# Kernel tuning notes

Measured on AMD Instinct MI355X. Metric: run time of the kernel, lower is better.

## Reference

```python
import jax, jax.numpy as jnp
import numpy as np

B, Te, Td, D_ENC, D_DEC, ATT = 8, 512, 128, 512, 512, 256


def setup_inputs() -> dict:
    key = jax.random.key(0)
    k0, k1, k2, k3, k4 = jax.random.split(key, 5)
    return {
        "values": jax.random.normal(k0, (B, Te, D_ENC), dtype=jnp.float32),
        "query": jax.random.normal(k1, (B, Td, D_DEC), dtype=jnp.float32),
        "W_h": jax.random.uniform(k2, (D_ENC, ATT), jnp.float32, -0.05, 0.05),
        "U_a": jax.random.uniform(k3, (D_DEC, ATT), jnp.float32, -0.05, 0.05),
        "V_a": jax.random.uniform(k4, (1, ATT), jnp.float32, -0.05, 0.05),
    }


def reference(values, query, W_h, U_a, V_a):
    # values: [B, Te, D_ENC] encoder output sequence (single entry in 'values' list)
    # query:  [B, Td, D_DEC] decoder output sequence
    # With a single encoder sequence, broadcast_sum/broadcast_concat reduces are identities.
    W_hi = jnp.einsum('bse,ea->bsa', values, W_h)        # [B, Te, ATT]
    U_a_dot_s = jnp.einsum('btd,da->bta', query, U_a)    # [B, Td, ATT]
    # tanh(h.Wa + s.Ua): vectorized over all decoder timesteps (K.rnn scan unrolled)
    act = jnp.tanh(W_hi[:, None, :, :] + U_a_dot_s[:, :, None, :])  # [B, Td, Te, ATT]
    scores = jnp.einsum('btsa,a->bts', act, V_a[0])      # [B, Td, Te]
    e_outputs = jax.nn.softmax(scores, axis=-1)          # softmax over encoder positions
    # context: weighted sum of encoder hidden states
    c_outputs = jnp.einsum('bts,bse->bte', e_outputs, values)  # [B, Td, D_ENC]
    return (c_outputs, e_outputs)
```

## Files before the change

### kernel.cpp

```cpp
#include <hip/hip_runtime.h>
#include <hip/hip_bf16.h>


typedef __attribute__((ext_vector_type(8))) short bf16x8;
typedef __attribute__((ext_vector_type(4))) float f32x4;

__device__ inline void f32_to_bf16_pair(float x, short& h, short& l) {
    unsigned u = __builtin_bit_cast(unsigned, x);
    unsigned r = u + 0x7FFFu + ((u >> 16) & 1u);
    h = (short)(r >> 16);
    float xh = __builtin_bit_cast(float, r & 0xFFFF0000u);
    float xl = x - xh;
    unsigned u2 = __builtin_bit_cast(unsigned, xl);
    unsigned r2 = u2 + 0x7FFFu + ((u2 >> 16) & 1u);
    l = (short)(r2 >> 16);
}

__global__ __launch_bounds__(256) void prep(
    const float* __restrict__ W_h, const float* __restrict__ U_a,
    const float* __restrict__ values, const float* __restrict__ query,
    short* __restrict__ BHi, short* __restrict__ BLo,
    short* __restrict__ AHi, short* __restrict__ ALo)
{
    __shared__ float TW[64][65];
    __shared__ float TA[16][516];
    const int bid = blockIdx.x;
    const int tid = threadIdx.x;

    if (bid < 64) {
        const int mat = bid >> 5, nb = (bid >> 3) & 3, kb = bid & 7;
        const float* W = mat ? U_a : W_h;
        {
            const int krow = tid >> 2, cq = (tid & 3) * 16;
            const float* src = W + (size_t)(kb * 64 + krow) * 256 + nb * 64 + cq;
            #pragma unroll
            for (int q = 0; q < 4; ++q)
                *(float4*)&TW[krow][cq + q * 4] = *(const float4*)&src[q * 4];
        }
        __syncthreads();
        {
            const int f = tid >> 5;
            const int ngl = f >> 1, ksl = f & 1;
            const int l0 = (tid & 31) * 2;
            const int ngrp = nb * 4 + ngl;
            const int ksg = kb * 2 + ksl;
            const size_t base = (size_t)mat * 131072 + ((size_t)(ngrp * 16 + ksg)) * 512;
            #pragma unroll
            for (int li = 0; li < 2; ++li) {
                const int lane = l0 + li;
                const int lr = lane & 15, lg = lane >> 4;
                bf16x8 hv, lv;
                #pragma unroll
                for (int j = 0; j < 8; ++j) {
                    short h, l;
                    f32_to_bf16_pair(TW[ksl * 32 + lg * 8 + j][ngl * 16 + lr], h, l);
                    hv[j] = h; lv[j] = l;
                }
                *(bf16x8*)(BHi + base + lane * 8) = hv;
                *(bf16x8*)(BLo + base + lane * 8) = lv;
            }
        }
    } else {
        const int mg = bid - 64;
        const float* src = (mg < 256) ? values + (size_t)mg * 16 * 512
                                      : query + (size_t)(mg - 256) * 16 * 512;
        {
            const int row = tid >> 4, c0 = (tid & 15) * 4;
            #pragma unroll
            for (int i = 0; i < 8; ++i)
                *(float4*)&TA[row][c0 + i * 64] =
                    *(const float4*)&src[(size_t)row * 512 + c0 + i * 64];
        }
        __syncthreads();
        {
            const int ks = tid >> 4;
            const int l4 = (tid & 15) * 4;
            const size_t base = ((size_t)(mg * 16 + ks)) * 512;
            #pragma unroll
            for (int li = 0; li < 4; ++li) {
                const int lane = l4 + li;
                const int lr = lane & 15, lg = lane >> 4;
                bf16x8 hv, lv;
                #pragma unroll
                for (int j = 0; j < 8; ++j) {
                    short h, l;
                    f32_to_bf16_pair(TA[lr][ks * 32 + lg * 8 + j], h, l);
                    hv[j] = h; lv[j] = l;
                }
                *(bf16x8*)(AHi + base + lane * 8) = hv;
                *(bf16x8*)(ALo + base + lane * 8) = lv;
            }
        }
    }
}

__global__ __launch_bounds__(128) void gemm_mfma(
    const short* __restrict__ AHi, const short* __restrict__ ALo,
    const short* __restrict__ BHi, const short* __restrict__ BLo,
    float* __restrict__ WhO, float* __restrict__ UO)
{
    const int bid = blockIdx.x;
    const int mt = bid >> 2, nt = bid & 3;
    const int tid = threadIdx.x;
    const int w = tid >> 6, l = tid & 63;
    const int lr = l & 15, lg = l >> 4;

    float* C; int m0, mg, matoff;
    if (mt < 128) { C = WhO; m0 = mt * 32; mg = mt * 2 + w; matoff = 0; }
    else { C = UO; m0 = (mt - 128) * 32; mg = 256 + (mt - 128) * 2 + w; matoff = 131072; }

    const short* ah_p = AHi + ((size_t)mg * 16) * 512 + l * 8;
    const short* al_p = ALo + ((size_t)mg * 16) * 512 + l * 8;
    const short* bh_p = BHi + matoff + ((size_t)(nt * 4) * 16) * 512 + l * 8;
    const short* bl_p = BLo + matoff + ((size_t)(nt * 4) * 16) * 512 + l * 8;

    f32x4 acc[4];
    #pragma unroll
    for (int nc = 0; nc < 4; ++nc) acc[nc] = (f32x4){0.f, 0.f, 0.f, 0.f};

    #pragma unroll 2
    for (int ks = 0; ks < 16; ++ks) {
        bf16x8 ah = *(const bf16x8*)(ah_p + (size_t)ks * 512);
        bf16x8 al = *(const bf16x8*)(al_p + (size_t)ks * 512);
        #pragma unroll
        for (int nc = 0; nc < 4; ++nc) {
            bf16x8 bh = *(const bf16x8*)(bh_p + ((size_t)(nc * 16 + ks)) * 512);
            bf16x8 bl = *(const bf16x8*)(bl_p + ((size_t)(nc * 16 + ks)) * 512);
            acc[nc] = __builtin_amdgcn_mfma_f32_16x16x32_bf16(ah, bh, acc[nc], 0, 0, 0);
            acc[nc] = __builtin_amdgcn_mfma_f32_16x16x32_bf16(al, bh, acc[nc], 0, 0, 0);
            acc[nc] = __builtin_amdgcn_mfma_f32_16x16x32_bf16(ah, bl, acc[nc], 0, 0, 0);
        }
    }

    const float SCL = 2.8853900817779268f;
    float* cp = C + (size_t)(m0 + w * 16 + lg * 4) * 256 + nt * 64 + lr;
    #pragma unroll
    for (int nc = 0; nc < 4; ++nc)
        #pragma unroll
        for (int r = 0; r < 4; ++r)
            cp[(size_t)r * 256 + nc * 16] = acc[nc][r] * SCL;
}

__global__ __launch_bounds__(256) void scores_k(
    const float* __restrict__ Whl, const float* __restrict__ Ul,
    const float* __restrict__ Va, float* __restrict__ scoresP)
{
    __shared__ float Ws[64][68];
    __shared__ float Us[16][68];

    const int bid = blockIdx.x;
    const int b = bid & 7;
    const int rest = bid >> 3;
    const int ah = rest & 3;
    const int tt = (rest >> 2) & 7;
    const int st = rest >> 5;
    const int t0 = tt * 16, s0 = st * 64, a0 = ah * 64;
    const int tid = threadIdx.x;

    {
        const int r = tid >> 2, c16 = (tid & 3) * 16;
        const float* wsrc = Whl + (size_t)(b * 512 + s0 + r) * 256 + a0 + c16;
        #pragma unroll
        for (int q = 0; q < 4; ++q)
            *(float4*)&Ws[r][c16 + q * 4] = *(const float4*)&wsrc[q * 4];
        const int r8 = tid >> 4, c8 = (tid & 15) * 4;
        const float* usrc = Ul + (size_t)(b * 128 + t0 + r8) * 256 + a0 + c8;
        *(float4*)&Us[r8][c8] = *(const float4*)&usrc[0];
    }
    __syncthreads();

    const int t = tid >> 4;
    const int ss = tid & 15;
    const float* Vp = Va + a0;

    float acc[4] = {};
    #pragma unroll 4
    for (int a = 0; a < 64; a += 4) {
        float4 u  = *(const float4*)&Us[t][a];
        float4 w0 = *(const float4*)&Ws[ss][a];
        float4 w1 = *(const float4*)&Ws[ss + 16][a];
        float4 w2 = *(const float4*)&Ws[ss + 32][a];
        float4 w3 = *(const float4*)&Ws[ss + 48][a];
        const float uv[4] = {u.x, u.y, u.z, u.w};
        const float wv[4][4] = {{w0.x, w0.y, w0.z, w0.w}, {w1.x, w1.y, w1.z, w1.w},
                                {w2.x, w2.y, w2.z, w2.w}, {w3.x, w3.y, w3.z, w3.w}};
        #pragma unroll
        for (int q = 0; q < 4; ++q) {
            const float vq = Vp[a + q];
            #pragma unroll
            for (int k = 0; k < 4; ++k) {
                float e = __builtin_amdgcn_exp2f(wv[k][q] + uv[q]);
                float r = __builtin_amdgcn_rcpf(1.f + e);
                acc[k] = fmaf(vq, r, acc[k]);
            }
        }
    }

    float* sp = scoresP + (size_t)ah * 524288
              + (size_t)(b * 128 + t0 + t) * 512 + s0 + ss;
    #pragma unroll
    for (int k = 0; k < 4; ++k) sp[k * 16] = acc[k];
}

__global__ __launch_bounds__(512) void softmax_ctx(
    const float* __restrict__ scoresP, const float* __restrict__ values,
    float* __restrict__ out_c, float* __restrict__ out_e)
{
    __shared__ float Ps[4][512];
    __shared__ float Part[7][4][256];

    const int bid = blockIdx.x;
    const int b = bid & 7;
    const int rest = bid >> 3;
    const int tg = rest & 31;
    const int eh = rest >> 5;
    const int t0 = tg * 4;
    const int tid = threadIdx.x;

    if (tid < 256) {
        const int row = tid >> 6, lane = tid & 63;
        const float* sp = scoresP + (size_t)(b * 128 + t0 + row) * 512;
        float e[8]; float ssum = 0.f;
        #pragma unroll
        for (int k = 0; k < 8; ++k) {
            const int idx = k * 64 + lane;
            float s = sp[idx] + sp[524288 + idx] + sp[1048576 + idx] + sp[1572864 + idx];
            e[k] = __builtin_amdgcn_exp2f(s * -2.8853900817779268f);
            ssum += e[k];
        }
        #pragma unroll
        for (int off = 32; off > 0; off >>= 1)
            ssum += __shfl_xor(ssum, off);
        const float inv = 1.0f / ssum;
        float* erow = out_e + (size_t)(b * 128 + t0 + row) * 512;
        #pragma unroll
        for (int k = 0; k < 8; ++k) {
            float p = e[k] * inv;
            Ps[row][k * 64 + lane] = p;
            if (eh == 0) erow[k * 64 + lane] = p;
        }
    }
    __syncthreads();

    const int el = (tid & 63) * 4;
    const int e4 = eh * 256 + el;
    const int sh = tid >> 6;
    const int sb = sh * 64;
    const float* vb = values + (size_t)b * 262144;

    float4 a0 = {0,0,0,0}, a1 = {0,0,0,0}, a2 = {0,0,0,0}, a3 = {0,0,0,0};
    #pragma unroll 2
    for (int s2 = 0; s2 < 64; s2 += 4) {
        float4 q0 = *(const float4*)&Ps[0][sb + s2];
        float4 q1 = *(const float4*)&Ps[1][sb + s2];
        float4 q2 = *(const float4*)&Ps[2][sb + s2];
        float4 q3 = *(const float4*)&Ps[3][sb + s2];
        const float q0v[4] = {q0.x, q0.y, q0.z, q0.w};
        const float q1v[4] = {q1.x, q1.y, q1.z, q1.w};
        const float q2v[4] = {q2.x, q2.y, q2.z, q2.w};
        const float q3v[4] = {q3.x, q3.y, q3.z, q3.w};
        #pragma unroll
        for (int j = 0; j < 4; ++j) {
            float4 v4 = *(const float4*)&vb[(size_t)(sb + s2 + j) * 512 + e4];
            a0.x = fmaf(q0v[j], v4.x, a0.x); a0.y = fmaf(q0v[j], v4.y, a0.y);
            a0.z = fmaf(q0v[j], v4.z, a0.z); a0.w = fmaf(q0v[j], v4.w, a0.w);
            a1.x = fmaf(q1v[j], v4.x, a1.x); a1.y = fmaf(q1v[j], v4.y, a1.y);
            a1.z = fmaf(q1v[j], v4.z, a1.z); a1.w = fmaf(q1v[j], v4.w, a1.w);
            a2.x = fmaf(q2v[j], v4.x, a2.x); a2.y = fmaf(q2v[j], v4.y, a2.y);
            a2.z = fmaf(q2v[j], v4.z, a2.z); a2.w = fmaf(q2v[j], v4.w, a2.w);
            a3.x = fmaf(q3v[j], v4.x, a3.x); a3.y = fmaf(q3v[j], v4.y, a3.y);
            a3.z = fmaf(q3v[j], v4.z, a3.z); a3.w = fmaf(q3v[j], v4.w, a3.w);
        }
    }

    if (sh) {
        *(float4*)&Part[sh - 1][0][el] = a0;
        *(float4*)&Part[sh - 1][1][el] = a1;
        *(float4*)&Part[sh - 1][2][el] = a2;
        *(float4*)&Part[sh - 1][3][el] = a3;
    }
    __syncthreads();
    if (!sh) {
        #pragma unroll
        for (int rrow = 0; rrow < 4; ++rrow) {
            float4 acc = (rrow == 0) ? a0 : (rrow == 1) ? a1 : (rrow == 2) ? a2 : a3;
            #pragma unroll
            for (int g = 0; g < 7; ++g) {
                float4 p4 = *(const float4*)&Part[g][rrow][el];
                acc.x += p4.x; acc.y += p4.y; acc.z += p4.z; acc.w += p4.w;
            }
            *(float4*)&out_c[(size_t)(b * 128 + t0 + rrow) * 512 + e4] = acc;
        }
    }
}

extern "C" void kernel_launch(void* const* d_in, const int* in_sizes, int n_in,
                              void* d_out, int out_size, void* d_ws, size_t ws_size,
                              hipStream_t stream) {
    const float* values = (const float*)d_in[0];
    const float* query  = (const float*)d_in[1];
    const float* W_h    = (const float*)d_in[2];
    const float* U_a    = (const float*)d_in[3];
    const float* V_a    = (const float*)d_in[4];

    float* ws      = (float*)d_ws;
    float* Whl     = ws;
    float* Ul      = ws + 1048576;
    float* scoresP = ws + 1310720;
    short* S       = (short*)(ws + 3407872);
    short* AHi     = S;
    short* ALo     = S + 2621440;
    short* BHi     = S + 5242880;
    short* BLo     = S + 5505024;

    float* out_c = (float*)d_out;
    float* out_e = out_c + 8 * 128 * 512;

    hipLaunchKernelGGL(prep, dim3(384), dim3(256), 0, stream,
                       W_h, U_a, values, query, BHi, BLo, AHi, ALo);
    hipLaunchKernelGGL(gemm_mfma, dim3(640), dim3(128), 0, stream,
                       AHi, ALo, BHi, BLo, Whl, Ul);
    hipLaunchKernelGGL(scores_k, dim3(2048), dim3(256), 0, stream,
                       Whl, Ul, V_a, scoresP);
    hipLaunchKernelGGL(softmax_ctx, dim3(512), dim3(512), 0, stream,
                       scoresP, values, out_c, out_e);
}
```

Measured before the change: 64.76 us.

## Fuse pipeline into cooperative persistent kernel and split A operand inside GEMM

Merges the four kernels into one cooperative persistent kernel with grid-wide syncs between phases, and falls back to separate launches if the cooperative launch fails. The GEMM no longer reads a prepacked bf16 hi/lo copy of values and query. It double-buffers the fp32 A tile through shared memory and splits it into bf16 hi/lo in registers with truncation, which removes the prep pass and its workspace traffic. The softmax-context phase now runs with 256 threads over half-width column slices across 1024 items. The change risks grid.sync overhead, lower occupancy from the union shared-memory footprint, and slightly different rounding from the truncating split.

Result: slower. 241.6 us (+273.1%).

```diff
diff --git a/kernel.cpp b/kernel.cpp
--- a/kernel.cpp
+++ b/kernel.cpp
@@ -1,5 +1,8 @@
 #include <hip/hip_runtime.h>
 #include <hip/hip_bf16.h>
+#include <hip/hip_cooperative_groups.h>
+
+namespace cg = cooperative_groups;
 
 
 typedef __attribute__((ext_vector_type(8))) short bf16x8;
@@ -16,120 +19,123 @@
     l = (short)(r2 >> 16);
 }
 
-__global__ __launch_bounds__(256) void prep(
+__device__ inline void split_trunc(float x, short& h, short& l) {
+    unsigned u = __builtin_bit_cast(unsigned, x);
+    h = (short)(u >> 16);
+    float xh = __builtin_bit_cast(float, u & 0xFFFF0000u);
+    unsigned u2 = __builtin_bit_cast(unsigned, x - xh);
+    l = (short)(u2 >> 16);
+}
+
+struct PwS { float TW[64][65]; };
+struct GmS { float As[2][64][68]; };
+struct ScS { float Ws[64][68]; float Us[16][68]; };
+struct SxS { float Ps[4][512]; float Part[7][4][128]; };
+union Smem { PwS pw; GmS gm; ScS sc; SxS sx; };
+
+__device__ void phase_prepB(int item, int tid, PwS& sm,
     const float* __restrict__ W_h, const float* __restrict__ U_a,
+    short* __restrict__ BHi, short* __restrict__ BLo)
+{
+    const int mat = item >> 5, nb = (item >> 3) & 3, kb = item & 7;
+    const float* W = mat ? U_a : W_h;
+    const int krow = tid >> 2, cq = (tid & 3) * 16;
+    const float* src = W + (size_t)(kb * 64 + krow) * 256 + nb * 64 + cq;
+    #pragma unroll
+    for (int q = 0; q < 4; ++q)
+        *(float4*)&sm.TW[krow][cq + q * 4] = *(const float4*)&src[q * 4];
+    __syncthreads();
+    const int f = tid >> 5;
+    const int ngl = f >> 1, ksl = f & 1;
+    const int l0 = (tid & 31) * 2;
+    const int ngrp = nb * 4 + ngl;
+    const int ksg = kb * 2 + ksl;
+    const size_t base = (size_t)mat * 131072 + (size_t)(ngrp * 16 + ksg) * 512;
+    #pragma unroll
+    for (int li = 0; li < 2; ++li) {
+        const int lane = l0 + li;
+        const int lr = lane & 15, lg = lane >> 4;
+        bf16x8 hv, lv;
+        #pragma unroll
+        for (int j = 0; j < 8; ++j) {
+            short h, l;
+            f32_to_bf16_pair(sm.TW[ksl * 32 + lg * 8 + j][ngl * 16 + lr], h, l);
+            hv[j] = h; lv[j] = l;
+        }
+        *(bf16x8*)(BHi + base + lane * 8) = hv;
+        *(bf16x8*)(BLo + base + lane * 8) = lv;
+    }
+    __syncthreads();
+}
+
+__device__ void phase_gemm(int item, int tid, GmS& sm,
     const float* __restrict__ values, const float* __restrict__ query,
-    short* __restrict__ BHi, short* __restrict__ BLo,
-    short* __restrict__ AHi, short* __restrict__ ALo)
-{
-    __shared__ float TW[64][65];
-    __shared__ float TA[16][516];
-    const int bid = blockIdx.x;
-    const int tid = threadIdx.x;
-
-    if (bid < 64) {
-        const int mat = bid >> 5, nb = (bid >> 3) & 3, kb = bid & 7;
-        const float* W = mat ? U_a : W_h;
-        {
-            const int krow = tid >> 2, cq = (tid & 3) * 16;
-            const float* src = W + (size_t)(kb * 64 + krow) * 256 + nb * 64 + cq;
-            #pragma unroll
-            for (int q = 0; q < 4; ++q)
-                *(float4*)&TW[krow][cq + q * 4] = *(const float4*)&src[q * 4];
-        }
-        __syncthreads();
-        {
-            const int f = tid >> 5;
-            const int ngl = f >> 1, ksl = f & 1;
-            const int l0 = (tid & 31) * 2;
-            const int ngrp = nb * 4 + ngl;
-            const int ksg = kb * 2 + ksl;
-            const size_t base = (size_t)mat * 131072 + ((size_t)(ngrp * 16 + ksg)) * 512;
-            #pragma unroll
-            for (int li = 0; li < 2; ++li) {
-                const int lane = l0 + li;
-                const int lr = lane & 15, lg = lane >> 4;
-                bf16x8 hv, lv;
-                #pragma unroll
-                for (int j = 0; j < 8; ++j) {
-                    short h, l;
-                    f32_to_bf16_pair(TW[ksl * 32 + lg * 8 + j][ngl * 16 + lr], h, l);
-                    hv[j] = h; lv[j] = l;
-                }
-                *(bf16x8*)(BHi + base + lane * 8) = hv;
-                *(bf16x8*)(BLo + base + lane * 8) = lv;
-            }
-        }
-    } else {
-        const int mg = bid - 64;
-        const float* src = (mg < 256) ? values + (size_t)mg * 16 * 512
-                                      : query + (size_t)(mg - 256) * 16 * 512;
-        {
-            const int row = tid >> 4, c0 = (tid & 15) * 4;
-            #pragma unroll
-            for (int i = 0; i < 8; ++i)
-                *(float4*)&TA[row][c0 + i * 64] =
-                    *(const float4*)&src[(size_t)row * 512 + c0 + i * 64];
-        }
-        __syncthreads();
-        {
-            const int ks = tid >> 4;
-            const int l4 = (tid & 15) * 4;
-            const size_t base = ((size_t)(mg * 16 + ks)) * 512;
-            #pragma unroll
-            for (int li = 0; li < 4; ++li) {
-                const int lane = l4 + li;
-                const int lr = lane & 15, lg = lane >> 4;
-                bf16x8 hv, lv;
-                #pragma unroll
-                for (int j = 0; j < 8; ++j) {
-                    short h, l;
-                    f32_to_bf16_pair(TA[lr][ks * 32 + lg * 8 + j], h, l);
-                    hv[j] = h; lv[j] = l;
-                }
-                *(bf16x8*)(AHi + base + lane * 8) = hv;
-                *(bf16x8*)(ALo + base + lane * 8) = lv;
-            }
-        }
-    }
-}
-
-__global__ __launch_bounds__(128) void gemm_mfma(
-    const short* __restrict__ AHi, const short* __restrict__ ALo,
     const short* __restrict__ BHi, const short* __restrict__ BLo,
-    float* __restrict__ WhO, float* __restrict__ UO)
-{
-    const int bid = blockIdx.x;
-    const int mt = bid >> 2, nt = bid & 3;
-    const int tid = threadIdx.x;
+    float* __restrict__ Whl, float* __restrict__ Ul)
+{
+    const int mt = item >> 2, nt = item & 3;
     const int w = tid >> 6, l = tid & 63;
     const int lr = l & 15, lg = l >> 4;
-
-    float* C; int m0, mg, matoff;
-    if (mt < 128) { C = WhO; m0 = mt * 32; mg = mt * 2 + w; matoff = 0; }
-    else { C = UO; m0 = (mt - 128) * 32; mg = 256 + (mt - 128) * 2 + w; matoff = 131072; }
-
-    const short* ah_p = AHi + ((size_t)mg * 16) * 512 + l * 8;
-    const short* al_p = ALo + ((size_t)mg * 16) * 512 + l * 8;
-    const short* bh_p = BHi + matoff + ((size_t)(nt * 4) * 16) * 512 + l * 8;
-    const short* bl_p = BLo + matoff + ((size_t)(nt * 4) * 16) * 512 + l * 8;
+    const float* A; float* C; int m0; size_t matoff;
+    if (mt < 64) { A = values; C = Whl; m0 = mt * 64; matoff = 0; }
+    else { A = query; C = Ul; m0 = (mt - 64) * 64; matoff = 131072; }
+
+    const int srow = tid >> 2;
+    const int skc = (tid & 3) * 16;
+    const float* abase = A + (size_t)(m0 + srow) * 512 + skc;
 
     f32x4 acc[4];
     #pragma unroll
     for (int nc = 0; nc < 4; ++nc) acc[nc] = (f32x4){0.f, 0.f, 0.f, 0.f};
 
-    #pragma unroll 2
-    for (int ks = 0; ks < 16; ++ks) {
-        bf16x8 ah = *(const bf16x8*)(ah_p + (size_t)ks * 512);
-        bf16x8 al = *(const bf16x8*)(al_p + (size_t)ks * 512);
+    float4 pre[4];
+    #pragma unroll
+    for (int q = 0; q < 4; ++q) pre[q] = *(const float4*)(abase + q * 4);
+    #pragma unroll
+    for (int q = 0; q < 4; ++q)
+        *(float4*)&sm.As[0][srow][skc + q * 4] = pre[q];
+    __syncthreads();
+
+    for (int c = 0; c < 8; ++c) {
+        const int cur = c & 1;
+        if (c < 7) {
+            #pragma unroll
+            for (int q = 0; q < 4; ++q)
+                pre[q] = *(const float4*)(abase + (c + 1) * 64 + q * 4);
+        }
+        bf16x8 ah[2], al[2];
+        #pragma unroll
+        for (int ks = 0; ks < 2; ++ks) {
+            const float* ar = &sm.As[cur][w * 16 + lr][ks * 32 + lg * 8];
+            float4 f0 = *(const float4*)ar;
+            float4 f1 = *(const float4*)(ar + 4);
+            float xs[8] = {f0.x, f0.y, f0.z, f0.w, f1.x, f1.y, f1.z, f1.w};
+            #pragma unroll
+            for (int j = 0; j < 8; ++j) {
+                short h, lo2;
+                split_trunc(xs[j], h, lo2);
+                ah[ks][j] = h; al[ks][j] = lo2;
+            }
+        }
         #pragma unroll
         for (int nc = 0; nc < 4; ++nc) {
-            bf16x8 bh = *(const bf16x8*)(bh_p + ((size_t)(nc * 16 + ks)) * 512);
-            bf16x8 bl = *(const bf16x8*)(bl_p + ((size_t)(nc * 16 + ks)) * 512);
-            acc[nc] = __builtin_amdgcn_mfma_f32_16x16x32_bf16(ah, bh, acc[nc], 0, 0, 0);
-            acc[nc] = __builtin_amdgcn_mfma_f32_16x16x32_bf16(al, bh, acc[nc], 0, 0, 0);
-            acc[nc] = __builtin_amdgcn_mfma_f32_16x16x32_bf16(ah, bl, acc[nc], 0, 0, 0);
-        }
+            #pragma unroll
+            for (int ks = 0; ks < 2; ++ks) {
+                const size_t boff = matoff
+                    + (size_t)((nt * 4 + nc) * 16 + (c * 2 + ks)) * 512 + l * 8;
+                bf16x8 bh = *(const bf16x8*)(BHi + boff);
+                bf16x8 bl = *(const bf16x8*)(BLo + boff);
+                acc[nc] = __builtin_amdgcn_mfma_f32_16x16x32_bf16(ah[ks], bh, acc[nc], 0, 0, 0);
+                acc[nc] = __builtin_amdgcn_mfma_f32_16x16x32_bf16(al[ks], bh, acc[nc], 0, 0, 0);
+                acc[nc] = __builtin_amdgcn_mfma_f32_16x16x32_bf16(ah[ks], bl, acc[nc], 0, 0, 0);
+            }
+        }
+        if (c < 7) {
+            #pragma unroll
+            for (int q = 0; q < 4; ++q)
+                *(float4*)&sm.As[cur ^ 1][srow][skc + q * 4] = pre[q];
+        }
+        __syncthreads();
     }
 
     const float SCL = 2.8853900817779268f;
@@ -141,32 +147,25 @@
             cp[(size_t)r * 256 + nc * 16] = acc[nc][r] * SCL;
 }
 
-__global__ __launch_bounds__(256) void scores_k(
+__device__ void phase_scores(int item, int tid, ScS& sm,
     const float* __restrict__ Whl, const float* __restrict__ Ul,
     const float* __restrict__ Va, float* __restrict__ scoresP)
 {
-    __shared__ float Ws[64][68];
-    __shared__ float Us[16][68];
-
-    const int bid = blockIdx.x;
-    const int b = bid & 7;
-    const int rest = bid >> 3;
+    const int b = item & 7;
+    const int rest = item >> 3;
     const int ah = rest & 3;
     const int tt = (rest >> 2) & 7;
     const int st = rest >> 5;
     const int t0 = tt * 16, s0 = st * 64, a0 = ah * 64;
-    const int tid = threadIdx.x;
-
-    {
-        const int r = tid >> 2, c16 = (tid & 3) * 16;
-        const float* wsrc = Whl + (size_t)(b * 512 + s0 + r) * 256 + a0 + c16;
-        #pragma unroll
-        for (int q = 0; q < 4; ++q)
-            *(float4*)&Ws[r][c16 + q * 4] = *(const float4*)&wsrc[q * 4];
-        const int r8 = tid >> 4, c8 = (tid & 15) * 4;
-        const float* usrc = Ul + (size_t)(b * 128 + t0 + r8) * 256 + a0 + c8;
-        *(float4*)&Us[r8][c8] = *(const float4*)&usrc[0];
-    }
+
+    const int r = tid >> 2, c16 = (tid & 3) * 16;
+    const float* wsrc = Whl + (size_t)(b * 512 + s0 + r) * 256 + a0 + c16;
+    #pragma unroll
+    for (int q = 0; q < 4; ++q)
+        *(float4*)&sm.Ws[r][c16 + q * 4] = *(const float4*)&wsrc[q * 4];
+    const int r8 = tid >> 4, c8 = (tid & 15) * 4;
+    const float* usrc = Ul + (size_t)(b * 128 + t0 + r8) * 256 + a0 + c8;
+    *(float4*)&sm.Us[r8][c8] = *(const float4*)&usrc[0];
     __syncthreads();
 
     const int t = tid >> 4;
@@ -176,11 +175,11 @@
     float acc[4] = {};
     #pragma unroll 4
     for (int a = 0; a < 64; a += 4) {
-        float4 u  = *(const float4*)&Us[t][a];
-        float4 w0 = *(const float4*)&Ws[ss][a];
-        float4 w1 = *(const float4*)&Ws[ss + 16][a];
-        float4 w2 = *(const float4*)&Ws[ss + 32][a];
-        float4 w3 = *(const float4*)&Ws[ss + 48][a];
+        float4 u  = *(const float4*)&sm.Us[t][a];
+        float4 w0 = *(const float4*)&sm.Ws[ss][a];
+        float4 w1 = *(const float4*)&sm.Ws[ss + 16][a];
+        float4 w2 = *(const float4*)&sm.Ws[ss + 32][a];
+        float4 w3 = *(const float4*)&sm.Ws[ss + 48][a];
         const float uv[4] = {u.x, u.y, u.z, u.w};
         const float wv[4][4] = {{w0.x, w0.y, w0.z, w0.w}, {w1.x, w1.y, w1.z, w1.w},
                                 {w2.x, w2.y, w2.z, w2.w}, {w3.x, w3.y, w3.z, w3.w}};
@@ -190,8 +189,8 @@
             #pragma unroll
             for (int k = 0; k < 4; ++k) {
                 float e = __builtin_amdgcn_exp2f(wv[k][q] + uv[q]);
-                float r = __builtin_amdgcn_rcpf(1.f + e);
-                acc[k] = fmaf(vq, r, acc[k]);
+                float rc = __builtin_amdgcn_rcpf(1.f + e);
+                acc[k] = fmaf(vq, rc, acc[k]);
             }
         }
     }
@@ -200,24 +199,20 @@
               + (size_t)(b * 128 + t0 + t) * 512 + s0 + ss;
     #pragma unroll
     for (int k = 0; k < 4; ++k) sp[k * 16] = acc[k];
-}
-
-__global__ __launch_bounds__(512) void softmax_ctx(
+    __syncthreads();
+}
+
+__device__ void phase_softctx(int item, int tid, SxS& sm,
     const float* __restrict__ scoresP, const float* __restrict__ values,
     float* __restrict__ out_c, float* __restrict__ out_e)
 {
-    __shared__ float Ps[4][512];
-    __shared__ float Part[7][4][256];
-
-    const int bid = blockIdx.x;
-    const int b = bid & 7;
-    const int rest = bid >> 3;
+    const int b = item & 7;
+    const int rest = item >> 3;
     const int tg = rest & 31;
     const int eh = rest >> 5;
     const int t0 = tg * 4;
-    const int tid = threadIdx.x;
-
-    if (tid < 256) {
+
+    {
         const int row = tid >> 6, lane = tid & 63;
         const float* sp = scoresP + (size_t)(b * 128 + t0 + row) * 512;
         float e[8]; float ssum = 0.f;
@@ -236,25 +231,25 @@
         #pragma unroll
         for (int k = 0; k < 8; ++k) {
             float p = e[k] * inv;
-            Ps[row][k * 64 + lane] = p;
+            sm.Ps[row][k * 64 + lane] = p;
             if (eh == 0) erow[k * 64 + lane] = p;
         }
     }
     __syncthreads();
 
-    const int el = (tid & 63) * 4;
-    const int e4 = eh * 256 + el;
-    const int sh = tid >> 6;
+    const int sh = tid >> 5;
+    const int el = (tid & 31) * 4;
+    const int e4 = eh * 128 + el;
     const int sb = sh * 64;
     const float* vb = values + (size_t)b * 262144;
 
     float4 a0 = {0,0,0,0}, a1 = {0,0,0,0}, a2 = {0,0,0,0}, a3 = {0,0,0,0};
     #pragma unroll 2
     for (int s2 = 0; s2 < 64; s2 += 4) {
-        float4 q0 = *(const float4*)&Ps[0][sb + s2];
-        float4 q1 = *(const float4*)&Ps[1][sb + s2];
-        float4 q2 = *(const float4*)&Ps[2][sb + s2];
-        float4 q3 = *(const float4*)&Ps[3][sb + s2];
+        float4 q0 = *(const float4*)&sm.Ps[0][sb + s2];
+        float4 q1 = *(const float4*)&sm.Ps[1][sb + s2];
+        float4 q2 = *(const float4*)&sm.Ps[2][sb + s2];
+        float4 q3 = *(const float4*)&sm.Ps[3][sb + s2];
         const float q0v[4] = {q0.x, q0.y, q0.z, q0.w};
         const float q1v[4] = {q1.x, q1.y, q1.z, q1.w};
         const float q2v[4] = {q2.x, q2.y, q2.z, q2.w};
@@ -274,10 +269,10 @@
     }
 
     if (sh) {
-        *(float4*)&Part[sh - 1][0][el] = a0;
-        *(float4*)&Part[sh - 1][1][el] = a1;
-        *(float4*)&Part[sh - 1][2][el] = a2;
-        *(float4*)&Part[sh - 1][3][el] = a3;
+        *(float4*)&sm.Part[sh - 1][0][el] = a0;
+        *(float4*)&sm.Part[sh - 1][1][el] = a1;
+        *(float4*)&sm.Part[sh - 1][2][el] = a2;
+        *(float4*)&sm.Part[sh - 1][3][el] = a3;
     }
     __syncthreads();
     if (!sh) {
@@ -286,12 +281,74 @@
             float4 acc = (rrow == 0) ? a0 : (rrow == 1) ? a1 : (rrow == 2) ? a2 : a3;
             #pragma unroll
             for (int g = 0; g < 7; ++g) {
-                float4 p4 = *(const float4*)&Part[g][rrow][el];
+                float4 p4 = *(const float4*)&sm.Part[g][rrow][el];
                 acc.x += p4.x; acc.y += p4.y; acc.z += p4.z; acc.w += p4.w;
             }
             *(float4*)&out_c[(size_t)(b * 128 + t0 + rrow) * 512 + e4] = acc;
         }
     }
+    __syncthreads();
+}
+
+__global__ __launch_bounds__(256, 4) void mega(
+    const float* __restrict__ values, const float* __restrict__ query,
+    const float* __restrict__ W_h, const float* __restrict__ U_a,
+    const float* __restrict__ Va,
+    float* __restrict__ Whl, float* __restrict__ Ul,
+    float* __restrict__ scoresP,
+    short* __restrict__ BHi, short* __restrict__ BLo,
+    float* __restrict__ out_c, float* __restrict__ out_e)
+{
+    cg::grid_group grid = cg::this_grid();
+    __shared__ Smem sm;
+    const int bid = blockIdx.x;
+    const int tid = threadIdx.x;
+    const int G = gridDim.x;
+
+    for (int it = bid; it < 64; it += G)
+        phase_prepB(it, tid, sm.pw, W_h, U_a, BHi, BLo);
+    grid.sync();
+    for (int it = bid; it < 320; it += G)
+        phase_gemm(it, tid, sm.gm, values, query, BHi, BLo, Whl, Ul);
+    grid.sync();
+    for (int it = bid; it < 2048; it += G)
+        phase_scores(it, tid, sm.sc, Whl, Ul, Va, scoresP);
+    grid.sync();
+    for (int it = bid; it < 1024; it += G)
+        phase_softctx(it, tid, sm.sx, scoresP, values, out_c, out_e);
+}
+
+__global__ __launch_bounds__(256) void k_prep(
+    const float* __restrict__ W_h, const float* __restrict__ U_a,
+    short* __restrict__ BHi, short* __restrict__ BLo)
+{
+    __shared__ PwS sm;
+    phase_prepB(blockIdx.x, threadIdx.x, sm, W_h, U_a, BHi, BLo);
+}
+
+__global__ __launch_bounds__(256, 2) void k_gemm(
+    const float* __restrict__ values, const float* __restrict__ query,
+    const short* __restrict__ BHi, const short* __restrict__ BLo,
+    float* __restrict__ Whl, float* __restrict__ Ul)
+{
+    __shared__ GmS sm;
+    phase_gemm(blockIdx.x, threadIdx.x, sm, values, query, BHi, BLo, Whl, Ul);
+}
+
+__global__ __launch_bounds__(256) void k_scores(
+    const float* __restrict__ Whl, const float* __restrict__ Ul,
+    const float* __restrict__ Va, float* __restrict__ scoresP)
+{
+    __shared__ ScS sm;
+    phase_scores(blockIdx.x, threadIdx.x, sm, Whl, Ul, Va, scoresP);
+}
+
+__global__ __launch_bounds__(256) void k_softctx(
+    const float* __restrict__ scoresP, const float* __restrict__ values,
+    float* __restrict__ out_c, float* __restrict__ out_e)
+{
+    __shared__ SxS sm;
+    phase_softctx(blockIdx.x, threadIdx.x, sm, scoresP, values, out_c, out_e);
 }
 
 extern "C" void kernel_launch(void* const* d_in, const int* in_sizes, int n_in,
@@ -307,21 +364,37 @@
     float* Whl     = ws;
     float* Ul      = ws + 1048576;
     float* scoresP = ws + 1310720;
-    short* S       = (short*)(ws + 3407872);
-    short* AHi     = S;
-    short* ALo     = S + 2621440;
-    short* BHi     = S + 5242880;
-    short* BLo     = S + 5505024;
+    short* BHi     = (short*)(ws + 3407872);
+    short* BLo     = BHi + 262144;
 
     float* out_c = (float*)d_out;
     float* out_e = out_c + 8 * 128 * 512;
 
-    hipLaunchKernelGGL(prep, dim3(384), dim3(256), 0, stream,
-                       W_h, U_a, values, query, BHi, BLo, AHi, ALo);
-    hipLaunchKernelGGL(gemm_mfma, dim3(640), dim3(128), 0, stream,
-                       AHi, ALo, BHi, BLo, Whl, Ul);
-    hipLaunchKernelGGL(scores_k, dim3(2048), dim3(256), 0, stream,
-                       Whl, Ul, V_a, scoresP);
-    hipLaunchKernelGGL(softmax_ctx, dim3(512), dim3(512), 0, stream,
-                       scoresP, values, out_c, out_e);
-}
+    int nb = 0;
+    hipError_t qe = hipOccupancyMaxActiveBlocksPerMultiprocessor(
+        &nb, (const void*)mega, 256, 0);
+    int G = (qe == hipSuccess && nb > 0) ? nb * 256 : 0;
+    if (G > 2048) G = 2048;
+
+    bool done = false;
+    if (G >= 256) {
+        void* args[] = {
+            (void*)&values, (void*)&query, (void*)&W_h, (void*)&U_a, (void*)&V_a,
+            (void*)&Whl, (void*)&Ul, (void*)&scoresP, (void*)&BHi, (void*)&BLo,
+            (void*)&out_c, (void*)&out_e
+        };
+        hipError_t e = hipLaunchCooperativeKernel((void*)mega, dim3(G), dim3(256),
+                                                  args, 0, stream);
+        done = (e == hipSuccess);
+    }
+    if (!done) {
+        hipLaunchKernelGGL(k_prep, dim3(64), dim3(256), 0, stream,
+                           W_h, U_a, BHi, BLo);
+        hipLaunchKernelGGL(k_gemm, dim3(320), dim3(256), 0, stream,
+                           values, query, BHi, BLo, Whl, Ul);
+        hipLaunchKernelGGL(k_scores, dim3(2048), dim3(256), 0, stream,
+                           Whl, Ul, V_a, scoresP);
+        hipLaunchKernelGGL(k_softctx, dim3(1024), dim3(256), 0, stream,
+                           scoresP, values, out_c, out_e);
+    }
+}
```

## Fuse activation bf16 split into GEMM with double-buffered LDS staging

Applied to the files above, without the earlier changes.

The prep kernel no longer converts values/query into hi/lo bf16 arrays. The GEMM now loads fp32 activation tiles into double-buffered shared memory and splits them on the fly with truncation. This removes a full write and re-read of the split activations in global memory. The GEMM tile grows to 64 rows with 256 threads, and the softmax/context kernel is reshaped to 1024 blocks of 256 threads with a smaller e-slice per block. Truncation instead of round-to-nearest for the hi part may slightly change precision.

After: 89.04 us. 1.37x slower.

```diff
diff --git a/kernel.cpp b/kernel.cpp
--- a/kernel.cpp
+++ b/kernel.cpp
@@ -16,120 +16,123 @@
     l = (short)(r2 >> 16);
 }
 
-__global__ __launch_bounds__(256) void prep(
+__device__ inline void split_trunc(float x, short& h, short& l) {
+    unsigned u = __builtin_bit_cast(unsigned, x);
+    h = (short)(u >> 16);
+    float xh = __builtin_bit_cast(float, u & 0xFFFF0000u);
+    unsigned u2 = __builtin_bit_cast(unsigned, x - xh);
+    l = (short)(u2 >> 16);
+}
+
+__global__ __launch_bounds__(256) void k_prep(
     const float* __restrict__ W_h, const float* __restrict__ U_a,
-    const float* __restrict__ values, const float* __restrict__ query,
-    short* __restrict__ BHi, short* __restrict__ BLo,
-    short* __restrict__ AHi, short* __restrict__ ALo)
+    short* __restrict__ BHi, short* __restrict__ BLo)
 {
     __shared__ float TW[64][65];
-    __shared__ float TA[16][516];
     const int bid = blockIdx.x;
     const int tid = threadIdx.x;
-
-    if (bid < 64) {
-        const int mat = bid >> 5, nb = (bid >> 3) & 3, kb = bid & 7;
-        const float* W = mat ? U_a : W_h;
-        {
-            const int krow = tid >> 2, cq = (tid & 3) * 16;
-            const float* src = W + (size_t)(kb * 64 + krow) * 256 + nb * 64 + cq;
-            #pragma unroll
-            for (int q = 0; q < 4; ++q)
-                *(float4*)&TW[krow][cq + q * 4] = *(const float4*)&src[q * 4];
-        }
-        __syncthreads();
-        {
-            const int f = tid >> 5;
-            const int ngl = f >> 1, ksl = f & 1;
-            const int l0 = (tid & 31) * 2;
-            const int ngrp = nb * 4 + ngl;
-            const int ksg = kb * 2 + ksl;
-            const size_t base = (size_t)mat * 131072 + ((size_t)(ngrp * 16 + ksg)) * 512;
-            #pragma unroll
-            for (int li = 0; li < 2; ++li) {
-                const int lane = l0 + li;
-                const int lr = lane & 15, lg = lane >> 4;
-                bf16x8 hv, lv;
-                #pragma unroll
-                for (int j = 0; j < 8; ++j) {
-                    short h, l;
-                    f32_to_bf16_pair(TW[ksl * 32 + lg * 8 + j][ngl * 16 + lr], h, l);
-                    hv[j] = h; lv[j] = l;
-                }
-                *(bf16x8*)(BHi + base + lane * 8) = hv;
-                *(bf16x8*)(BLo + base + lane * 8) = lv;
-            }
-        }
-    } else {
-        const int mg = bid - 64;
-        const float* src = (mg < 256) ? values + (size_t)mg * 16 * 512
-                                      : query + (size_t)(mg - 256) * 16 * 512;
-        {
-            const int row = tid >> 4, c0 = (tid & 15) * 4;
-            #pragma unroll
-            for (int i = 0; i < 8; ++i)
-                *(float4*)&TA[row][c0 + i * 64] =
-                    *(const float4*)&src[(size_t)row * 512 + c0 + i * 64];
-        }
-        __syncthreads();
-        {
-            const int ks = tid >> 4;
-            const int l4 = (tid & 15) * 4;
-            const size_t base = ((size_t)(mg * 16 + ks)) * 512;
-            #pragma unroll
-            for (int li = 0; li < 4; ++li) {
-                const int lane = l4 + li;
-                const int lr = lane & 15, lg = lane >> 4;
-                bf16x8 hv, lv;
-                #pragma unroll
-                for (int j = 0; j < 8; ++j) {
-                    short h, l;
-                    f32_to_bf16_pair(TA[lr][ks * 32 + lg * 8 + j], h, l);
-                    hv[j] = h; lv[j] = l;
-                }
-                *(bf16x8*)(AHi + base + lane * 8) = hv;
-                *(bf16x8*)(ALo + base + lane * 8) = lv;
-            }
-        }
-    }
-}
-
-__global__ __launch_bounds__(128) void gemm_mfma(
-    const short* __restrict__ AHi, const short* __restrict__ ALo,
+    const int mat = bid >> 5, nb = (bid >> 3) & 3, kb = bid & 7;
+    const float* W = mat ? U_a : W_h;
+    const int krow = tid >> 2, cq = (tid & 3) * 16;
+    const float* src = W + (size_t)(kb * 64 + krow) * 256 + nb * 64 + cq;
+    #pragma unroll
+    for (int q = 0; q < 4; ++q)
+        *(float4*)&TW[krow][cq + q * 4] = *(const float4*)&src[q * 4];
+    __syncthreads();
+    const int f = tid >> 5;
+    const int ngl = f >> 1, ksl = f & 1;
+    const int l0 = (tid & 31) * 2;
+    const int ngrp = nb * 4 + ngl;
+    const int ksg = kb * 2 + ksl;
+    const size_t base = (size_t)mat * 131072 + (size_t)(ngrp * 16 + ksg) * 512;
+    #pragma unroll
+    for (int li = 0; li < 2; ++li) {
+        const int lane = l0 + li;
+        const int lr = lane & 15, lg = lane >> 4;
+        bf16x8 hv, lv;
+        #pragma unroll
+        for (int j = 0; j < 8; ++j) {
+            short h, l;
+            f32_to_bf16_pair(TW[ksl * 32 + lg * 8 + j][ngl * 16 + lr], h, l);
+            hv[j] = h; lv[j] = l;
+        }
+        *(bf16x8*)(BHi + base + lane * 8) = hv;
+        *(bf16x8*)(BLo + base + lane * 8) = lv;
+    }
+}
+
+__global__ __launch_bounds__(256) void k_gemm(
+    const float* __restrict__ values, const float* __restrict__ query,
     const short* __restrict__ BHi, const short* __restrict__ BLo,
-    float* __restrict__ WhO, float* __restrict__ UO)
+    float* __restrict__ Whl, float* __restrict__ Ul)
 {
+    __shared__ float As[2][64][68];
+
     const int bid = blockIdx.x;
     const int mt = bid >> 2, nt = bid & 3;
     const int tid = threadIdx.x;
     const int w = tid >> 6, l = tid & 63;
     const int lr = l & 15, lg = l >> 4;
-
-    float* C; int m0, mg, matoff;
-    if (mt < 128) { C = WhO; m0 = mt * 32; mg = mt * 2 + w; matoff = 0; }
-    else { C = UO; m0 = (mt - 128) * 32; mg = 256 + (mt - 128) * 2 + w; matoff = 131072; }
-
-    const short* ah_p = AHi + ((size_t)mg * 16) * 512 + l * 8;
-    const short* al_p = ALo + ((size_t)mg * 16) * 512 + l * 8;
-    const short* bh_p = BHi + matoff + ((size_t)(nt * 4) * 16) * 512 + l * 8;
-    const short* bl_p = BLo + matoff + ((size_t)(nt * 4) * 16) * 512 + l * 8;
+    const float* A; float* C; int m0; size_t matoff;
+    if (mt < 64) { A = values; C = Whl; m0 = mt * 64; matoff = 0; }
+    else { A = query; C = Ul; m0 = (mt - 64) * 64; matoff = 131072; }
+
+    const int srow = tid >> 2;
+    const int skc = (tid & 3) * 16;
+    const float* abase = A + (size_t)(m0 + srow) * 512 + skc;
 
     f32x4 acc[4];
     #pragma unroll
     for (int nc = 0; nc < 4; ++nc) acc[nc] = (f32x4){0.f, 0.f, 0.f, 0.f};
 
-    #pragma unroll 2
-    for (int ks = 0; ks < 16; ++ks) {
-        bf16x8 ah = *(const bf16x8*)(ah_p + (size_t)ks * 512);
-        bf16x8 al = *(const bf16x8*)(al_p + (size_t)ks * 512);
+    float4 pre[4];
+    #pragma unroll
+    for (int q = 0; q < 4; ++q) pre[q] = *(const float4*)(abase + q * 4);
+    #pragma unroll
+    for (int q = 0; q < 4; ++q)
+        *(float4*)&As[0][srow][skc + q * 4] = pre[q];
+    __syncthreads();
+
+    for (int c = 0; c < 8; ++c) {
+        const int cur = c & 1;
+        if (c < 7) {
+            #pragma unroll
+            for (int q = 0; q < 4; ++q)
+                pre[q] = *(const float4*)(abase + (c + 1) * 64 + q * 4);
+        }
+        bf16x8 ah[2], al[2];
+        #pragma unroll
+        for (int ks = 0; ks < 2; ++ks) {
+            const float* ar = &As[cur][w * 16 + lr][ks * 32 + lg * 8];
+            float4 f0 = *(const float4*)ar;
+            float4 f1 = *(const float4*)(ar + 4);
+            float xs[8] = {f0.x, f0.y, f0.z, f0.w, f1.x, f1.y, f1.z, f1.w};
+            #pragma unroll
+            for (int j = 0; j < 8; ++j) {
+                short h, lo2;
+                split_trunc(xs[j], h, lo2);
+                ah[ks][j] = h; al[ks][j] = lo2;
+            }
+        }
         #pragma unroll
         for (int nc = 0; nc < 4; ++nc) {
-            bf16x8 bh = *(const bf16x8*)(bh_p + ((size_t)(nc * 16 + ks)) * 512);
-            bf16x8 bl = *(const bf16x8*)(bl_p + ((size_t)(nc * 16 + ks)) * 512);
-            acc[nc] = __builtin_amdgcn_mfma_f32_16x16x32_bf16(ah, bh, acc[nc], 0, 0, 0);
-            acc[nc] = __builtin_amdgcn_mfma_f32_16x16x32_bf16(al, bh, acc[nc], 0, 0, 0);
-            acc[nc] = __builtin_amdgcn_mfma_f32_16x16x32_bf16(ah, bl, acc[nc], 0, 0, 0);
-        }
+            #pragma unroll
+            for (int ks = 0; ks < 2; ++ks) {
+                const size_t boff = matoff
+                    + (size_t)((nt * 4 + nc) * 16 + (c * 2 + ks)) * 512 + l * 8;
+                bf16x8 bh = *(const bf16x8*)(BHi + boff);
+                bf16x8 bl = *(const bf16x8*)(BLo + boff);
+                acc[nc] = __builtin_amdgcn_mfma_f32_16x16x32_bf16(ah[ks], bh, acc[nc], 0, 0, 0);
+                acc[nc] = __builtin_amdgcn_mfma_f32_16x16x32_bf16(al[ks], bh, acc[nc], 0, 0, 0);
+                acc[nc] = __builtin_amdgcn_mfma_f32_16x16x32_bf16(ah[ks], bl, acc[nc], 0, 0, 0);
+            }
+        }
+        if (c < 7) {
+            #pragma unroll
+            for (int q = 0; q < 4; ++q)
+                *(float4*)&As[cur ^ 1][srow][skc + q * 4] = pre[q];
+        }
+        __syncthreads();
     }
 
     const float SCL = 2.8853900817779268f;
@@ -141,7 +144,7 @@
             cp[(size_t)r * 256 + nc * 16] = acc[nc][r] * SCL;
 }
 
-__global__ __launch_bounds__(256) void scores_k(
+__global__ __launch_bounds__(256) void k_scores(
     const float* __restrict__ Whl, const float* __restrict__ Ul,
     const float* __restrict__ Va, float* __restrict__ scoresP)
 {
@@ -157,16 +160,14 @@
     const int t0 = tt * 16, s0 = st * 64, a0 = ah * 64;
     const int tid = threadIdx.x;
 
-    {
-        const int r = tid >> 2, c16 = (tid & 3) * 16;
-        const float* wsrc = Whl + (size_t)(b * 512 + s0 + r) * 256 + a0 + c16;
-        #pragma unroll
-        for (int q = 0; q < 4; ++q)
-            *(float4*)&Ws[r][c16 + q * 4] = *(const float4*)&wsrc[q * 4];
-        const int r8 = tid >> 4, c8 = (tid & 15) * 4;
-        const float* usrc = Ul + (size_t)(b * 128 + t0 + r8) * 256 + a0 + c8;
-        *(float4*)&Us[r8][c8] = *(const float4*)&usrc[0];
-    }
+    const int r = tid >> 2, c16 = (tid & 3) * 16;
+    const float* wsrc = Whl + (size_t)(b * 512 + s0 + r) * 256 + a0 + c16;
+    #pragma unroll
+    for (int q = 0; q < 4; ++q)
+        *(float4*)&Ws[r][c16 + q * 4] = *(const float4*)&wsrc[q * 4];
+    const int r8 = tid >> 4, c8 = (tid & 15) * 4;
+    const float* usrc = Ul + (size_t)(b * 128 + t0 + r8) * 256 + a0 + c8;
+    *(float4*)&Us[r8][c8] = *(const float4*)&usrc[0];
     __syncthreads();
 
     const int t = tid >> 4;
@@ -190,8 +191,8 @@
             #pragma unroll
             for (int k = 0; k < 4; ++k) {
                 float e = __builtin_amdgcn_exp2f(wv[k][q] + uv[q]);
-                float r = __builtin_amdgcn_rcpf(1.f + e);
-                acc[k] = fmaf(vq, r, acc[k]);
+                float rc = __builtin_amdgcn_rcpf(1.f + e);
+                acc[k] = fmaf(vq, rc, acc[k]);
             }
         }
     }
@@ -202,12 +203,12 @@
     for (int k = 0; k < 4; ++k) sp[k * 16] = acc[k];
 }
 
-__global__ __launch_bounds__(512) void softmax_ctx(
+__global__ __launch_bounds__(256) void k_softctx(
     const float* __restrict__ scoresP, const float* __restrict__ values,
     float* __restrict__ out_c, float* __restrict__ out_e)
 {
     __shared__ float Ps[4][512];
-    __shared__ float Part[7][4][256];
+    __shared__ float Part[7][4][128];
 
     const int bid = blockIdx.x;
     const int b = bid & 7;
@@ -217,7 +218,7 @@
     const int t0 = tg * 4;
     const int tid = threadIdx.x;
 
-    if (tid < 256) {
+    {
         const int row = tid >> 6, lane = tid & 63;
         const float* sp = scoresP + (size_t)(b * 128 + t0 + row) * 512;
         float e[8]; float ssum = 0.f;
@@ -242,9 +243,9 @@
     }
     __syncthreads();
 
-    const int el = (tid & 63) * 4;
-    const int e4 = eh * 256 + el;
-    const int sh = tid >> 6;
+    const int sh = tid >> 5;
+    const int el = (tid & 31) * 4;
+    const int e4 = eh * 128 + el;
     const int sb = sh * 64;
     const float* vb = values + (size_t)b * 262144;
 
@@ -307,21 +308,18 @@
     float* Whl     = ws;
     float* Ul      = ws + 1048576;
     float* scoresP = ws + 1310720;
-    short* S       = (short*)(ws + 3407872);
-    short* AHi     = S;
-    short* ALo     = S + 2621440;
-    short* BHi     = S + 5242880;
-    short* BLo     = S + 5505024;
+    short* BHi     = (short*)(ws + 3407872);
+    short* BLo     = BHi + 262144;
 
     float* out_c = (float*)d_out;
     float* out_e = out_c + 8 * 128 * 512;
 
-    hipLaunchKernelGGL(prep, dim3(384), dim3(256), 0, stream,
-                       W_h, U_a, values, query, BHi, BLo, AHi, ALo);
-    hipLaunchKernelGGL(gemm_mfma, dim3(640), dim3(128), 0, stream,
-                       AHi, ALo, BHi, BLo, Whl, Ul);
-    hipLaunchKernelGGL(scores_k, dim3(2048), dim3(256), 0, stream,
+    hipLaunchKernelGGL(k_prep, dim3(64), dim3(256), 0, stream,
+                       W_h, U_a, BHi, BLo);
+    hipLaunchKernelGGL(k_gemm, dim3(320), dim3(256), 0, stream,
+                       values, query, BHi, BLo, Whl, Ul);
+    hipLaunchKernelGGL(k_scores, dim3(2048), dim3(256), 0, stream,
                        Whl, Ul, V_a, scoresP);
-    hipLaunchKernelGGL(softmax_ctx, dim3(512), dim3(512), 0, stream,
+    hipLaunchKernelGGL(k_softctx, dim3(1024), dim3(256), 0, stream,
                        scoresP, values, out_c, out_e);
 }
```

## Precompute exponentials in GEMM epilogue and split softmax-context over more blocks

Applied to the files above, without the earlier changes.

The GEMM epilogue now stores exp2 of the scaled projections, so the scores kernel computes exp(a+b) as a product and no longer runs exp2 in its innermost B*Td*Te*ATT loop, leaving only a reciprocal. Separately, the softmax/context kernel goes from 512 blocks of 512 threads to 1024 blocks of 256 threads, each covering 128 output columns instead of 256. The product form risks overflow to inf for large activations, where rcp then yields 0, which matches tanh saturation. Each block still recomputes the softmax, now twice as often.

After: 58.20 us. 1.11x faster.

```diff
diff --git a/kernel.cpp b/kernel.cpp
--- a/kernel.cpp
+++ b/kernel.cpp
@@ -44,7 +44,7 @@
             const int l0 = (tid & 31) * 2;
             const int ngrp = nb * 4 + ngl;
             const int ksg = kb * 2 + ksl;
-            const size_t base = (size_t)mat * 131072 + ((size_t)(ngrp * 16 + ksg)) * 512;
+            const size_t base = (size_t)mat * 131072 + (size_t)(ngrp * 16 + ksg) * 512;
             #pragma unroll
             for (int li = 0; li < 2; ++li) {
                 const int lane = l0 + li;
@@ -97,7 +97,7 @@
 __global__ __launch_bounds__(128) void gemm_mfma(
     const short* __restrict__ AHi, const short* __restrict__ ALo,
     const short* __restrict__ BHi, const short* __restrict__ BLo,
-    float* __restrict__ WhO, float* __restrict__ UO)
+    float* __restrict__ EwO, float* __restrict__ EuO)
 {
     const int bid = blockIdx.x;
     const int mt = bid >> 2, nt = bid & 3;
@@ -106,8 +106,8 @@
     const int lr = l & 15, lg = l >> 4;
 
     float* C; int m0, mg, matoff;
-    if (mt < 128) { C = WhO; m0 = mt * 32; mg = mt * 2 + w; matoff = 0; }
-    else { C = UO; m0 = (mt - 128) * 32; mg = 256 + (mt - 128) * 2 + w; matoff = 131072; }
+    if (mt < 128) { C = EwO; m0 = mt * 32; mg = mt * 2 + w; matoff = 0; }
+    else { C = EuO; m0 = (mt - 128) * 32; mg = 256 + (mt - 128) * 2 + w; matoff = 131072; }
 
     const short* ah_p = AHi + ((size_t)mg * 16) * 512 + l * 8;
     const short* al_p = ALo + ((size_t)mg * 16) * 512 + l * 8;
@@ -138,11 +138,11 @@
     for (int nc = 0; nc < 4; ++nc)
         #pragma unroll
         for (int r = 0; r < 4; ++r)
-            cp[(size_t)r * 256 + nc * 16] = acc[nc][r] * SCL;
+            cp[(size_t)r * 256 + nc * 16] = __builtin_amdgcn_exp2f(acc[nc][r] * SCL);
 }
 
 __global__ __launch_bounds__(256) void scores_k(
-    const float* __restrict__ Whl, const float* __restrict__ Ul,
+    const float* __restrict__ Ew, const float* __restrict__ Eu,
     const float* __restrict__ Va, float* __restrict__ scoresP)
 {
     __shared__ float Ws[64][68];
@@ -157,16 +157,14 @@
     const int t0 = tt * 16, s0 = st * 64, a0 = ah * 64;
     const int tid = threadIdx.x;
 
-    {
-        const int r = tid >> 2, c16 = (tid & 3) * 16;
-        const float* wsrc = Whl + (size_t)(b * 512 + s0 + r) * 256 + a0 + c16;
-        #pragma unroll
-        for (int q = 0; q < 4; ++q)
-            *(float4*)&Ws[r][c16 + q * 4] = *(const float4*)&wsrc[q * 4];
-        const int r8 = tid >> 4, c8 = (tid & 15) * 4;
-        const float* usrc = Ul + (size_t)(b * 128 + t0 + r8) * 256 + a0 + c8;
-        *(float4*)&Us[r8][c8] = *(const float4*)&usrc[0];
-    }
+    const int r = tid >> 2, c16 = (tid & 3) * 16;
+    const float* wsrc = Ew + (size_t)(b * 512 + s0 + r) * 256 + a0 + c16;
+    #pragma unroll
+    for (int q = 0; q < 4; ++q)
+        *(float4*)&Ws[r][c16 + q * 4] = *(const float4*)&wsrc[q * 4];
+    const int r8 = tid >> 4, c8 = (tid & 15) * 4;
+    const float* usrc = Eu + (size_t)(b * 128 + t0 + r8) * 256 + a0 + c8;
+    *(float4*)&Us[r8][c8] = *(const float4*)&usrc[0];
     __syncthreads();
 
     const int t = tid >> 4;
@@ -189,9 +187,9 @@
             const float vq = Vp[a + q];
             #pragma unroll
             for (int k = 0; k < 4; ++k) {
-                float e = __builtin_amdgcn_exp2f(wv[k][q] + uv[q]);
-                float r = __builtin_amdgcn_rcpf(1.f + e);
-                acc[k] = fmaf(vq, r, acc[k]);
+                float e = wv[k][q] * uv[q];
+                float rc = __builtin_amdgcn_rcpf(1.f + e);
+                acc[k] = fmaf(vq, rc, acc[k]);
             }
         }
     }
@@ -202,12 +200,12 @@
     for (int k = 0; k < 4; ++k) sp[k * 16] = acc[k];
 }
 
-__global__ __launch_bounds__(512) void softmax_ctx(
+__global__ __launch_bounds__(256) void softctx(
     const float* __restrict__ scoresP, const float* __restrict__ values,
     float* __restrict__ out_c, float* __restrict__ out_e)
 {
     __shared__ float Ps[4][512];
-    __shared__ float Part[7][4][256];
+    __shared__ float Part[7][4][128];
 
     const int bid = blockIdx.x;
     const int b = bid & 7;
@@ -217,7 +215,7 @@
     const int t0 = tg * 4;
     const int tid = threadIdx.x;
 
-    if (tid < 256) {
+    {
         const int row = tid >> 6, lane = tid & 63;
         const float* sp = scoresP + (size_t)(b * 128 + t0 + row) * 512;
         float e[8]; float ssum = 0.f;
@@ -242,9 +240,9 @@
     }
     __syncthreads();
 
-    const int el = (tid & 63) * 4;
-    const int e4 = eh * 256 + el;
-    const int sh = tid >> 6;
+    const int sh = tid >> 5;
+    const int el = (tid & 31) * 4;
+    const int e4 = eh * 128 + el;
     const int sb = sh * 64;
     const float* vb = values + (size_t)b * 262144;
 
@@ -304,8 +302,8 @@
     const float* V_a    = (const float*)d_in[4];
 
     float* ws      = (float*)d_ws;
-    float* Whl     = ws;
-    float* Ul      = ws + 1048576;
+    float* Ew      = ws;
+    float* Eu      = ws + 1048576;
     float* scoresP = ws + 1310720;
     short* S       = (short*)(ws + 3407872);
     short* AHi     = S;
@@ -319,9 +317,9 @@
     hipLaunchKernelGGL(prep, dim3(384), dim3(256), 0, stream,
                        W_h, U_a, values, query, BHi, BLo, AHi, ALo);
     hipLaunchKernelGGL(gemm_mfma, dim3(640), dim3(128), 0, stream,
-                       AHi, ALo, BHi, BLo, Whl, Ul);
+                       AHi, ALo, BHi, BLo, Ew, Eu);
     hipLaunchKernelGGL(scores_k, dim3(2048), dim3(256), 0, stream,
-                       Whl, Ul, V_a, scoresP);
-    hipLaunchKernelGGL(softmax_ctx, dim3(512), dim3(512), 0, stream,
+                       Ew, Eu, V_a, scoresP);
+    hipLaunchKernelGGL(softctx, dim3(1024), dim3(256), 0, stream,
                        scoresP, values, out_c, out_e);
 }
```
